# Performance work log

Hardware: AMD Instinct MI355X
Metric: run time of the kernel (lower is better)

The kernel has to match this reference:

```python
import jax, jax.numpy as jnp
import numpy as np

B, S, D, H = 2, 2048, 1024, 16
DH = D // H  # key_dim = embed_dim // num_heads
NEG = 1e9    # Keras masked-softmax adder magnitude
EPS = 1e-6


def setup_inputs() -> dict:
    key = jax.random.key(0)
    ks = jax.random.split(key, 6)
    sc = 1.0 / np.sqrt(D)
    return {
        "x": jax.random.normal(ks[0], (B, S, D), jnp.float32),
        "Wq": jax.random.normal(ks[1], (D, H, DH), jnp.float32) * sc,
        "bq": jnp.zeros((H, DH), jnp.float32),
        "Wk": jax.random.normal(ks[2], (D, H, DH), jnp.float32) * sc,
        "bk": jnp.zeros((H, DH), jnp.float32),
        "Wv": jax.random.normal(ks[3], (D, H, DH), jnp.float32) * sc,
        "bv": jnp.zeros((H, DH), jnp.float32),
        "Wo": jax.random.normal(ks[4], (H, DH, D), jnp.float32) * (1.0 / np.sqrt(D)),
        "bo": jnp.zeros((D,), jnp.float32),
        "gamma": jnp.ones((D,), jnp.float32),
        "beta": jnp.zeros((D,), jnp.float32),
    }


def reference(x, Wq, bq, Wk, bk, Wv, bv, Wo, bo, gamma, beta):
    # Keras MultiHeadAttention(query=x, value=x), inference (dropouts are identity)
    q = jnp.einsum("bsd,dhk->bshk", x, Wq) + bq  # [B,S,H,DH]
    k = jnp.einsum("bsd,dhk->bshk", x, Wk) + bk
    v = jnp.einsum("bsd,dhk->bshk", x, Wv) + bv

    scores = jnp.einsum("bqhd,bkhd->bhqk", q, k) / jnp.sqrt(jnp.asarray(DH, x.dtype))
    # Source: mask = 1 - band_part(ones, -1, 0) -> ones strictly ABOVE diagonal.
    # Keras attends where mask==1 and adds (1-mask)*(-1e9) elsewhere. Faithful:
    i = jnp.arange(S)[:, None]
    j = jnp.arange(S)[None, :]
    allowed = (j > i).astype(scores.dtype)  # [S,S], strict upper triangle
    scores = scores + (allowed - 1.0) * NEG  # subtract 1e9 where not allowed
    probs = jax.nn.softmax(scores, axis=-1)

    ctx = jnp.einsum("bhqk,bkhd->bqhd", probs, v)  # [B,S,H,DH]
    attn_out = jnp.einsum("bqhd,hdo->bqo", ctx, Wo) + bo  # [B,S,D]

    # residual + LayerNorm(eps=1e-6)
    y = x + attn_out
    mu = jnp.mean(y, axis=-1, keepdims=True)
    var = jnp.mean(jnp.square(y - mu), axis=-1, keepdims=True)
    return (y - mu) * jax.lax.rsqrt(var + EPS) * gamma + beta
```

## Files before the change

kernel.cpp:

```cpp
#include <hip/hip_runtime.h>
#include <hip/hip_bf16.h>

typedef __hip_bfloat16 bf16;
typedef __attribute__((ext_vector_type(8))) short bf16x8;
typedef __attribute__((ext_vector_type(4))) float f32x4;

constexpr int Bc  = 2;
constexpr int Sc  = 2048;
constexpr int Dc  = 1024;
constexpr int Hc  = 16;
constexpr int DHc = 64;
constexpr int BS  = Bc * Sc;
constexpr int NT  = Sc / 64;

__device__ __forceinline__ float bs2f(unsigned short u) {
    union { unsigned int i; float f; } v; v.i = ((unsigned int)u) << 16; return v.f;
}
__device__ __forceinline__ short f2bs(float x) {
    bf16 h = __float2bfloat16(x);
    return *reinterpret_cast<short*>(&h);
}

typedef const __attribute__((address_space(1))) unsigned int* as1_u32p;
typedef __attribute__((address_space(3))) unsigned int* as3_u32p;
__device__ __forceinline__ void gl_lds16(const void* g, void* l) {
    __builtin_amdgcn_global_load_lds((as1_u32p)g, (as3_u32p)l, 16, 0, 0);
}

__global__ __launch_bounds__(256) void cast_x(const float* __restrict__ in,
                                              short* __restrict__ out) {
    const int i = (blockIdx.x * 256 + threadIdx.x) * 4;
    const float4 v = *(const float4*)(in + i);
    ushort4 o;
    o.x = (unsigned short)f2bs(v.x);
    o.y = (unsigned short)f2bs(v.y);
    o.z = (unsigned short)f2bs(v.z);
    o.w = (unsigned short)f2bs(v.w);
    *(ushort4*)(out + i) = o;
}

__global__ __launch_bounds__(256) void transpose_cast(
    const float* __restrict__ w0, const float* __restrict__ w1,
    const float* __restrict__ w2, const float* __restrict__ w3,
    short* __restrict__ outbase)
{
    __shared__ float T[64][65];
    const int z = blockIdx.z;
    const float* in = (z == 0) ? w0 : (z == 1) ? w1 : (z == 2) ? w2 : w3;
    short* out = outbase + (size_t)z * 1024 * 1024;
    const int k0 = blockIdx.x * 64, n0 = blockIdx.y * 64;
    const int t = threadIdx.x;
    #pragma unroll
    for (int it = 0; it < 4; ++it) {
        const int s = it * 256 + t;
        const int r = s >> 4, c = (s & 15) * 4;
        *(float4*)&T[r][c] = *(const float4*)(in + (size_t)(k0 + r) * 1024 + n0 + c);
    }
    __syncthreads();
    #pragma unroll
    for (int it = 0; it < 4; ++it) {
        const int s = it * 256 + t;
        const int rr = s >> 4, cc = (s & 15) * 4;
        ushort4 o;
        o.x = (unsigned short)f2bs(T[cc + 0][rr]);
        o.y = (unsigned short)f2bs(T[cc + 1][rr]);
        o.z = (unsigned short)f2bs(T[cc + 2][rr]);
        o.w = (unsigned short)f2bs(T[cc + 3][rr]);
        *(ushort4*)(out + (size_t)(n0 + rr) * 1024 + k0 + cc) = o;
    }
}

__global__ __launch_bounds__(256, 2) void gemm_bt(
    const short* __restrict__ A, const short* __restrict__ BTbase,
    const float* __restrict__ b0, const float* __restrict__ b1,
    const float* __restrict__ b2, short* __restrict__ Cbase)
{
    __shared__ __align__(16) short As[128 * 64];
    __shared__ __align__(16) short Bs[128 * 64];

    const int z = blockIdx.z;
    const short* BT = BTbase + (size_t)z * 1024 * 1024;
    const float* bias = (z == 0) ? b0 : (z == 1) ? b1 : b2;
    short* C = Cbase + (size_t)z * BS * Dc;

    const int t = threadIdx.x;
    const int lane = t & 63, w = t >> 6;
    const int quad = lane >> 4, l16 = lane & 15;
    const int wm = (w & 1) * 64, wn = (w >> 1) * 64;
    const int row0 = blockIdx.y * 128;
    const int col0 = blockIdx.x * 128;
    const int sw = l16 & 7;

    f32x4 acc[4][4] = {};

    for (int kt = 0; kt < 1024; kt += 64) {
        __syncthreads();
        #pragma unroll
        for (int i = 0; i < 4; ++i) {
            const int f = i * 256 + t;
            const int r = f >> 3;
            const int g = (f & 7) ^ (r & 7);
            short* lb = &As[(i * 256 + w * 64) * 8];
            gl_lds16(A + (size_t)(row0 + r) * 1024 + kt + g * 8, lb);
            short* lb2 = &Bs[(i * 256 + w * 64) * 8];
            gl_lds16(BT + (size_t)(col0 + r) * 1024 + kt + g * 8, lb2);
        }
        __syncthreads();
        #pragma unroll
        for (int ks = 0; ks < 2; ++ks) {
            bf16x8 av[4], bv[4];
            #pragma unroll
            for (int mt = 0; mt < 4; ++mt) {
                const int r = wm + mt * 16 + l16;
                av[mt] = *(const bf16x8*)&As[r * 64 + ((ks * 4 + quad) ^ sw) * 8];
            }
            #pragma unroll
            for (int nt = 0; nt < 4; ++nt) {
                const int r = wn + nt * 16 + l16;
                bv[nt] = *(const bf16x8*)&Bs[r * 64 + ((ks * 4 + quad) ^ sw) * 8];
            }
            #pragma unroll
            for (int mt = 0; mt < 4; ++mt)
                #pragma unroll
                for (int nt = 0; nt < 4; ++nt)
                    acc[mt][nt] = __builtin_amdgcn_mfma_f32_16x16x32_bf16(
                        av[mt], bv[nt], acc[mt][nt], 0, 0, 0);
        }
    }

    float bvv[4];
    #pragma unroll
    for (int nt = 0; nt < 4; ++nt) bvv[nt] = bias[col0 + wn + nt * 16 + l16];
    #pragma unroll
    for (int mt = 0; mt < 4; ++mt)
        #pragma unroll
        for (int reg = 0; reg < 4; ++reg) {
            const size_t row = row0 + wm + mt * 16 + quad * 4 + reg;
            #pragma unroll
            for (int nt = 0; nt < 4; ++nt) {
                const int col = col0 + wn + nt * 16 + l16;
                C[row * 1024 + col] = f2bs(acc[mt][nt][reg] + bvv[nt]);
            }
        }
}

__device__ __forceinline__ void qtile_step(
    const bf16x8 (&qf)[2], const bf16x8 (&kf)[2][4],
    const short (&VsT)[64][72], short (&Psw)[16][72],
    const int k0, const int row_base,
    const int quad, const int l16,
    float (&l)[4], f32x4 (&O)[4])
{
    f32x4 S[4] = {};
    #pragma unroll
    for (int ks = 0; ks < 2; ++ks)
        #pragma unroll
        for (int nt = 0; nt < 4; ++nt)
            S[nt] = __builtin_amdgcn_mfma_f32_16x16x32_bf16(qf[ks], kf[ks][nt], S[nt], 0, 0, 0);

    #pragma unroll
    for (int nt = 0; nt < 4; ++nt) {
        const int col = k0 + nt * 16 + l16;
        #pragma unroll
        for (int reg = 0; reg < 4; ++reg) {
            const int row = row_base + quad * 4 + reg;
            const float s = (col > row) ? fminf(S[nt][reg] * 0.125f, 80.f) : -87.0f;
            const float p = __expf(s);
            S[nt][reg] = p;
            l[reg] += p;
        }
    }

    #pragma unroll
    for (int nt = 0; nt < 4; ++nt)
        #pragma unroll
        for (int reg = 0; reg < 4; ++reg)
            Psw[quad * 4 + reg][nt * 16 + l16] = f2bs(S[nt][reg]);

    #pragma unroll
    for (int ks = 0; ks < 2; ++ks) {
        const bf16x8 pf = *(const bf16x8*)&Psw[l16][ks * 32 + quad * 8];
        #pragma unroll
        for (int nt = 0; nt < 4; ++nt) {
            const bf16x8 vf = *(const bf16x8*)&VsT[nt * 16 + l16][ks * 32 + quad * 8];
            O[nt] = __builtin_amdgcn_mfma_f32_16x16x32_bf16(pf, vf, O[nt], 0, 0, 0);
        }
    }
}

__global__ __launch_bounds__(256, 2) void attn_mfma(
    const short* __restrict__ Qg, const short* __restrict__ Kg,
    const short* __restrict__ Vg, short* __restrict__ CTX)
{
    __shared__ __align__(16) short Ks [64][72];
    __shared__ __align__(16) short VsT[64][72];
    __shared__ __align__(16) short Ps[4][16][72];

    const int tid  = threadIdx.x;
    const int lane = tid & 63, w = tid >> 6;
    const int quad = lane >> 4, l16 = lane & 15;
    const int p  = blockIdx.x;
    const int h  = blockIdx.y;
    const int b  = blockIdx.z;
    const size_t rb = (size_t)b * Sc;
    const int cb = h * DHc;

    const int qa0 = p * 64;
    const int qb0 = (NT - 1 - p) * 64;
    const int tA0 = p;
    const int tB0 = NT - 1 - p;

    bf16x8 qfA[2], qfB[2];
    {
        const short* qa = Qg + (rb + qa0 + w * 16 + l16) * (size_t)Dc + cb + quad * 8;
        qfA[0] = *(const bf16x8*)(qa);
        qfA[1] = *(const bf16x8*)(qa + 32);
        const short* qb = Qg + (rb + qb0 + w * 16 + l16) * (size_t)Dc + cb + quad * 8;
        qfB[0] = *(const bf16x8*)(qb);
        qfB[1] = *(const bf16x8*)(qb + 32);
    }

    float lA[4] = {}, lB[4] = {};
    f32x4 OA[4] = {}, OB[4] = {};

    const int skey = tid & 63, sseg = (tid >> 6) * 16;

    {
        const size_t g = (rb + tA0 * 64 + skey) * (size_t)Dc + cb + sseg;
        const bf16x8 k0v = *(const bf16x8*)(Kg + g);
        const bf16x8 k1v = *(const bf16x8*)(Kg + g + 8);
        const bf16x8 v0v = *(const bf16x8*)(Vg + g);
        const bf16x8 v1v = *(const bf16x8*)(Vg + g + 8);
        *(bf16x8*)&Ks[skey][sseg]     = k0v;
        *(bf16x8*)&Ks[skey][sseg + 8] = k1v;
        #pragma unroll
        for (int e = 0; e < 8; ++e) {
            VsT[sseg + e][skey]     = v0v[e];
            VsT[sseg + 8 + e][skey] = v1v[e];
        }
    }
    __syncthreads();

    for (int t = tA0; t < NT; ++t) {
        const bool havenext = (t + 1 < NT);
        bf16x8 pk0, pk1, pv0, pv1;
        if (havenext) {
            const size_t g = (rb + (t + 1) * 64 + skey) * (size_t)Dc + cb + sseg;
            pk0 = *(const bf16x8*)(Kg + g);
            pk1 = *(const bf16x8*)(Kg + g + 8);
            pv0 = *(const bf16x8*)(Vg + g);
            pv1 = *(const bf16x8*)(Vg + g + 8);
        }

        const int k0 = t * 64;
        bf16x8 kf[2][4];
        #pragma unroll
        for (int ks = 0; ks < 2; ++ks)
            #pragma unroll
            for (int nt = 0; nt < 4; ++nt)
                kf[ks][nt] = *(const bf16x8*)&Ks[nt * 16 + l16][ks * 32 + quad * 8];

        qtile_step(qfA, kf, VsT, Ps[w], k0, qa0 + w * 16, quad, l16, lA, OA);
        if (t >= tB0)
            qtile_step(qfB, kf, VsT, Ps[w], k0, qb0 + w * 16, quad, l16, lB, OB);

        if (havenext) {
            __syncthreads();
            *(bf16x8*)&Ks[skey][sseg]     = pk0;
            *(bf16x8*)&Ks[skey][sseg + 8] = pk1;
            #pragma unroll
            for (int e = 0; e < 8; ++e) {
                VsT[sseg + e][skey]     = pv0[e];
                VsT[sseg + 8 + e][skey] = pv1[e];
            }
            __syncthreads();
        }
    }

    #pragma unroll
    for (int off = 1; off < 16; off <<= 1)
        #pragma unroll
        for (int reg = 0; reg < 4; ++reg) {
            lA[reg] += __shfl_xor(lA[reg], off, 64);
            lB[reg] += __shfl_xor(lB[reg], off, 64);
        }
    #pragma unroll
    for (int reg = 0; reg < 4; ++reg) { lA[reg] = 1.0f / lA[reg]; lB[reg] = 1.0f / lB[reg]; }
    #pragma unroll
    for (int nt = 0; nt < 4; ++nt)
        #pragma unroll
        for (int reg = 0; reg < 4; ++reg) {
            const size_t ra = rb + qa0 + w * 16 + quad * 4 + reg;
            CTX[ra * Dc + cb + nt * 16 + l16] = f2bs(OA[nt][reg] * lA[reg]);
            const size_t rbq = rb + qb0 + w * 16 + quad * 4 + reg;
            CTX[rbq * Dc + cb + nt * 16 + l16] = f2bs(OB[nt][reg] * lB[reg]);
        }
}

__global__ __launch_bounds__(256) void vmean(const short* __restrict__ V,
                                             short* __restrict__ CTX)
{
    const int h = blockIdx.x, b = blockIdx.y;
    const int t = threadIdx.x;
    const int dh = t & 63, ck = t >> 6;
    float s = 0.f;
    const short* vp = V + ((size_t)b * Sc + ck * 512) * Dc + h * DHc + dh;
    for (int j = 0; j < 512; ++j) s += bs2f(vp[(size_t)j * Dc]);
    __shared__ float red[4][64];
    red[ck][dh] = s;
    __syncthreads();
    if (ck == 0) {
        const float tot = (red[0][dh] + red[1][dh] + red[2][dh] + red[3][dh]) * (1.f / Sc);
        CTX[((size_t)b * Sc + Sc - 1) * Dc + h * DHc + dh] = f2bs(tot);
    }
}

__global__ __launch_bounds__(256, 4) void resid_ln(
    const float* __restrict__ X, const short* __restrict__ AO,
    const float* __restrict__ gamma, const float* __restrict__ beta,
    float* __restrict__ out)
{
    const int r = blockIdx.x;
    const int t = threadIdx.x;
    const size_t base = (size_t)r * Dc + t * 4;

    const float4 x4 = *(const float4*)(X + base);
    const ushort4 a4 = *(const ushort4*)(AO + base);
    float y[4];
    y[0] = x4.x + bs2f(a4.x);
    y[1] = x4.y + bs2f(a4.y);
    y[2] = x4.z + bs2f(a4.z);
    y[3] = x4.w + bs2f(a4.w);

    float s  = y[0] + y[1] + y[2] + y[3];
    float s2 = y[0]*y[0] + y[1]*y[1] + y[2]*y[2] + y[3]*y[3];
    #pragma unroll
    for (int off = 1; off < 64; off <<= 1) {
        s  += __shfl_xor(s,  off, 64);
        s2 += __shfl_xor(s2, off, 64);
    }
    __shared__ float red[8];
    const int w = t >> 6;
    if ((t & 63) == 0) { red[w] = s; red[4 + w] = s2; }
    __syncthreads();
    s  = red[0] + red[1] + red[2] + red[3];
    s2 = red[4] + red[5] + red[6] + red[7];

    const float mu   = s * (1.0f / Dc);
    const float rstd = rsqrtf(s2 * (1.0f / Dc) - mu * mu + 1e-6f);

    const float4 g4 = *(const float4*)(gamma + t * 4);
    const float4 b4 = *(const float4*)(beta  + t * 4);
    float4 o;
    o.x = (y[0] - mu) * rstd * g4.x + b4.x;
    o.y = (y[1] - mu) * rstd * g4.y + b4.y;
    o.z = (y[2] - mu) * rstd * g4.z + b4.z;
    o.w = (y[3] - mu) * rstd * g4.w + b4.w;
    *(float4*)(out + base) = o;
}

extern "C" void kernel_launch(void* const* d_in, const int* in_sizes, int n_in,
                              void* d_out, int out_size, void* d_ws, size_t ws_size,
                              hipStream_t stream)
{
    (void)in_sizes; (void)n_in; (void)out_size; (void)ws_size;
    const float* x     = (const float*)d_in[0];
    const float* Wq    = (const float*)d_in[1];
    const float* bq    = (const float*)d_in[2];
    const float* Wk    = (const float*)d_in[3];
    const float* bk    = (const float*)d_in[4];
    const float* Wv    = (const float*)d_in[5];
    const float* bv    = (const float*)d_in[6];
    const float* Wo    = (const float*)d_in[7];
    const float* bo    = (const float*)d_in[8];
    const float* gamma = (const float*)d_in[9];
    const float* beta  = (const float*)d_in[10];
    float* out = (float*)d_out;

    const size_t matN = (size_t)BS * Dc;
    const size_t wN   = (size_t)Dc * Dc;
    short* xb = (short*)d_ws;
    short* WT = xb + matN;
    short* Qb = WT + 4 * wN;
    short* Kb = Qb + matN;
    short* Vb = Kb + matN;
    short* Cx = Vb + matN;
    short* AO = Qb;

    cast_x<<<matN / 1024, 256, 0, stream>>>(x, xb);

    dim3 gt(16, 16, 4);
    transpose_cast<<<gt, 256, 0, stream>>>(Wq, Wk, Wv, Wo, WT);

    dim3 gq(Dc / 128, BS / 128, 3);
    gemm_bt<<<gq, 256, 0, stream>>>(xb, WT, bq, bk, bv, Qb);

    dim3 ga(16, Hc, Bc);
    attn_mfma<<<ga, 256, 0, stream>>>(Qb, Kb, Vb, Cx);

    dim3 gv(Hc, Bc);
    vmean<<<gv, 256, 0, stream>>>(Vb, Cx);

    dim3 go(Dc / 128, BS / 128, 1);
    gemm_bt<<<go, 256, 0, stream>>>(Cx, WT + 3 * wN, bo, bo, bo, AO);

    resid_ln<<<BS, 256, 0, stream>>>(x, AO, gamma, beta, out);
}
```

Before: 227.5 us.

## Split paired attention query tiles across 8 waves and raise GEMM occupancy hint

Result: no change. 225.2 us (-1.0%).

```diff
diff --git a/kernel.cpp b/kernel.cpp
--- a/kernel.cpp
+++ b/kernel.cpp
@@ -70,7 +70,7 @@
     }
 }
 
-__global__ __launch_bounds__(256, 2) void gemm_bt(
+__global__ __launch_bounds__(256, 3) void gemm_bt(
     const short* __restrict__ A, const short* __restrict__ BTbase,
     const float* __restrict__ b0, const float* __restrict__ b1,
     const float* __restrict__ b2, short* __restrict__ Cbase)
@@ -188,91 +188,74 @@
     }
 }
 
-__global__ __launch_bounds__(256, 2) void attn_mfma(
+__global__ __launch_bounds__(512, 4) void attn_mfma(
     const short* __restrict__ Qg, const short* __restrict__ Kg,
     const short* __restrict__ Vg, short* __restrict__ CTX)
 {
     __shared__ __align__(16) short Ks [64][72];
     __shared__ __align__(16) short VsT[64][72];
-    __shared__ __align__(16) short Ps[4][16][72];
+    __shared__ __align__(16) short Ps[8][16][72];
 
     const int tid  = threadIdx.x;
     const int lane = tid & 63, w = tid >> 6;
     const int quad = lane >> 4, l16 = lane & 15;
+    const int wq   = w & 3;
+    const bool isA = (w < 4);
     const int p  = blockIdx.x;
     const int h  = blockIdx.y;
     const int b  = blockIdx.z;
     const size_t rb = (size_t)b * Sc;
     const int cb = h * DHc;
 
-    const int qa0 = p * 64;
-    const int qb0 = (NT - 1 - p) * 64;
-    const int tA0 = p;
-    const int tB0 = NT - 1 - p;
-
-    bf16x8 qfA[2], qfB[2];
+    const int myT0 = isA ? p : (NT - 1 - p);
+    const int q0   = myT0 * 64;
+
+    bf16x8 qf[2];
     {
-        const short* qa = Qg + (rb + qa0 + w * 16 + l16) * (size_t)Dc + cb + quad * 8;
-        qfA[0] = *(const bf16x8*)(qa);
-        qfA[1] = *(const bf16x8*)(qa + 32);
-        const short* qb = Qg + (rb + qb0 + w * 16 + l16) * (size_t)Dc + cb + quad * 8;
-        qfB[0] = *(const bf16x8*)(qb);
-        qfB[1] = *(const bf16x8*)(qb + 32);
-    }
-
-    float lA[4] = {}, lB[4] = {};
-    f32x4 OA[4] = {}, OB[4] = {};
-
-    const int skey = tid & 63, sseg = (tid >> 6) * 16;
+        const short* qp = Qg + (rb + q0 + wq * 16 + l16) * (size_t)Dc + cb + quad * 8;
+        qf[0] = *(const bf16x8*)(qp);
+        qf[1] = *(const bf16x8*)(qp + 32);
+    }
+
+    float l[4] = {};
+    f32x4 O[4] = {};
+
+    const int skey = tid & 63, sseg = (tid >> 6) * 8;
 
     {
-        const size_t g = (rb + tA0 * 64 + skey) * (size_t)Dc + cb + sseg;
-        const bf16x8 k0v = *(const bf16x8*)(Kg + g);
-        const bf16x8 k1v = *(const bf16x8*)(Kg + g + 8);
-        const bf16x8 v0v = *(const bf16x8*)(Vg + g);
-        const bf16x8 v1v = *(const bf16x8*)(Vg + g + 8);
-        *(bf16x8*)&Ks[skey][sseg]     = k0v;
-        *(bf16x8*)&Ks[skey][sseg + 8] = k1v;
-        #pragma unroll
-        for (int e = 0; e < 8; ++e) {
-            VsT[sseg + e][skey]     = v0v[e];
-            VsT[sseg + 8 + e][skey] = v1v[e];
-        }
+        const size_t g = (rb + p * 64 + skey) * (size_t)Dc + cb + sseg;
+        const bf16x8 kv = *(const bf16x8*)(Kg + g);
+        const bf16x8 vv = *(const bf16x8*)(Vg + g);
+        *(bf16x8*)&Ks[skey][sseg] = kv;
+        #pragma unroll
+        for (int e = 0; e < 8; ++e) VsT[sseg + e][skey] = vv[e];
     }
     __syncthreads();
 
-    for (int t = tA0; t < NT; ++t) {
+    for (int t = p; t < NT; ++t) {
         const bool havenext = (t + 1 < NT);
-        bf16x8 pk0, pk1, pv0, pv1;
+        bf16x8 pk, pv;
         if (havenext) {
             const size_t g = (rb + (t + 1) * 64 + skey) * (size_t)Dc + cb + sseg;
-            pk0 = *(const bf16x8*)(Kg + g);
-            pk1 = *(const bf16x8*)(Kg + g + 8);
-            pv0 = *(const bf16x8*)(Vg + g);
-            pv1 = *(const bf16x8*)(Vg + g + 8);
-        }
-
-        const int k0 = t * 64;
-        bf16x8 kf[2][4];
-        #pragma unroll
-        for (int ks = 0; ks < 2; ++ks)
-            #pragma unroll
-            for (int nt = 0; nt < 4; ++nt)
-                kf[ks][nt] = *(const bf16x8*)&Ks[nt * 16 + l16][ks * 32 + quad * 8];
-
-        qtile_step(qfA, kf, VsT, Ps[w], k0, qa0 + w * 16, quad, l16, lA, OA);
-        if (t >= tB0)
-            qtile_step(qfB, kf, VsT, Ps[w], k0, qb0 + w * 16, quad, l16, lB, OB);
+            pk = *(const bf16x8*)(Kg + g);
+            pv = *(const bf16x8*)(Vg + g);
+        }
+
+        if (t >= myT0) {
+            bf16x8 kf[2][4];
+            #pragma unroll
+            for (int ks = 0; ks < 2; ++ks)
+                #pragma unroll
+                for (int nt = 0; nt < 4; ++nt)
+                    kf[ks][nt] = *(const bf16x8*)&Ks[nt * 16 + l16][ks * 32 + quad * 8];
+            qtile_step(qf, kf, VsT, Ps[w], t * 64, q0 + wq * 16, quad, l16, l, O);
+        }
 
         if (havenext) {
             __syncthreads();
-            *(bf16x8*)&Ks[skey][sseg]     = pk0;
-            *(bf16x8*)&Ks[skey][sseg + 8] = pk1;
-            #pragma unroll
-            for (int e = 0; e < 8; ++e) {
-                VsT[sseg + e][skey]     = pv0[e];
-                VsT[sseg + 8 + e][skey] = pv1[e];
-            }
+            *(bf16x8*)&Ks[skey][sseg] = pk;
+            #pragma unroll
+            for (int e = 0; e < 8; ++e) VsT[sseg + e][skey] = pv[e];
             __syncthreads();
         }
     }
@@ -280,20 +263,16 @@
     #pragma unroll
     for (int off = 1; off < 16; off <<= 1)
         #pragma unroll
+        for (int reg = 0; reg < 4; ++reg)
+            l[reg] += __shfl_xor(l[reg], off, 64);
+    #pragma unroll
+    for (int reg = 0; reg < 4; ++reg) l[reg] = 1.0f / l[reg];
+    #pragma unroll
+    for (int nt = 0; nt < 4; ++nt)
+        #pragma unroll
         for (int reg = 0; reg < 4; ++reg) {
-            lA[reg] += __shfl_xor(lA[reg], off, 64);
-            lB[reg] += __shfl_xor(lB[reg], off, 64);
-        }
-    #pragma unroll
-    for (int reg = 0; reg < 4; ++reg) { lA[reg] = 1.0f / lA[reg]; lB[reg] = 1.0f / lB[reg]; }
-    #pragma unroll
-    for (int nt = 0; nt < 4; ++nt)
-        #pragma unroll
-        for (int reg = 0; reg < 4; ++reg) {
-            const size_t ra = rb + qa0 + w * 16 + quad * 4 + reg;
-            CTX[ra * Dc + cb + nt * 16 + l16] = f2bs(OA[nt][reg] * lA[reg]);
-            const size_t rbq = rb + qb0 + w * 16 + quad * 4 + reg;
-            CTX[rbq * Dc + cb + nt * 16 + l16] = f2bs(OB[nt][reg] * lB[reg]);
+            const size_t row = rb + q0 + wq * 16 + quad * 4 + reg;
+            CTX[row * Dc + cb + nt * 16 + l16] = f2bs(O[nt][reg] * l[reg]);
         }
 }
 
@@ -396,7 +375,7 @@
     gemm_bt<<<gq, 256, 0, stream>>>(xb, WT, bq, bk, bv, Qb);
 
     dim3 ga(16, Hc, Bc);
-    attn_mfma<<<ga, 256, 0, stream>>>(Qb, Kb, Vb, Cx);
+    attn_mfma<<<ga, 512, 0, stream>>>(Qb, Kb, Vb, Cx);
 
     dim3 gv(Hc, Bc);
     vmean<<<gv, 256, 0, stream>>>(Vb, Cx);
```

## Split attention key range across two blocks and combine partial outputs

Applied to the files above, without the earlier changes.

Result: slower. 249.2 us (+9.6%).

```diff
diff --git a/kernel.cpp b/kernel.cpp
--- a/kernel.cpp
+++ b/kernel.cpp
@@ -70,7 +70,7 @@
     }
 }
 
-__global__ __launch_bounds__(256, 2) void gemm_bt(
+__global__ __launch_bounds__(256, 3) void gemm_bt(
     const short* __restrict__ A, const short* __restrict__ BTbase,
     const float* __restrict__ b0, const float* __restrict__ b1,
     const float* __restrict__ b2, short* __restrict__ Cbase)
@@ -188,9 +188,11 @@
     }
 }
 
-__global__ __launch_bounds__(256, 2) void attn_mfma(
+__global__ __launch_bounds__(256, 4) void attn_split(
     const short* __restrict__ Qg, const short* __restrict__ Kg,
-    const short* __restrict__ Vg, short* __restrict__ CTX)
+    const short* __restrict__ Vg,
+    short* __restrict__ Pa, short* __restrict__ Pb,
+    float* __restrict__ l0, float* __restrict__ l1)
 {
     __shared__ __align__(16) short Ks [64][72];
     __shared__ __align__(16) short VsT[64][72];
@@ -199,102 +201,120 @@
     const int tid  = threadIdx.x;
     const int lane = tid & 63, w = tid >> 6;
     const int quad = lane >> 4, l16 = lane & 15;
-    const int p  = blockIdx.x;
+    const int qs   = blockIdx.x >> 1;
+    const int half = blockIdx.x & 1;
     const int h  = blockIdx.y;
     const int b  = blockIdx.z;
     const size_t rb = (size_t)b * Sc;
     const int cb = h * DHc;
 
-    const int qa0 = p * 64;
-    const int qb0 = (NT - 1 - p) * 64;
-    const int tA0 = p;
-    const int tB0 = NT - 1 - p;
-
-    bf16x8 qfA[2], qfB[2];
+    const int q0 = qs * 64;
+    const int n  = NT - qs;
+    const int h0 = (n + 1) >> 1;
+    const int t_begin = half ? (qs + h0) : qs;
+    const int t_end   = half ? NT : (qs + h0);
+    short* Pout = half ? Pb : Pa;
+    float* lout = half ? l1 : l0;
+
+    bf16x8 qf[2];
     {
-        const short* qa = Qg + (rb + qa0 + w * 16 + l16) * (size_t)Dc + cb + quad * 8;
-        qfA[0] = *(const bf16x8*)(qa);
-        qfA[1] = *(const bf16x8*)(qa + 32);
-        const short* qb = Qg + (rb + qb0 + w * 16 + l16) * (size_t)Dc + cb + quad * 8;
-        qfB[0] = *(const bf16x8*)(qb);
-        qfB[1] = *(const bf16x8*)(qb + 32);
-    }
-
-    float lA[4] = {}, lB[4] = {};
-    f32x4 OA[4] = {}, OB[4] = {};
+        const short* qp = Qg + (rb + q0 + w * 16 + l16) * (size_t)Dc + cb + quad * 8;
+        qf[0] = *(const bf16x8*)(qp);
+        qf[1] = *(const bf16x8*)(qp + 32);
+    }
+
+    float l[4] = {};
+    f32x4 O[4] = {};
 
     const int skey = tid & 63, sseg = (tid >> 6) * 16;
 
-    {
-        const size_t g = (rb + tA0 * 64 + skey) * (size_t)Dc + cb + sseg;
-        const bf16x8 k0v = *(const bf16x8*)(Kg + g);
-        const bf16x8 k1v = *(const bf16x8*)(Kg + g + 8);
-        const bf16x8 v0v = *(const bf16x8*)(Vg + g);
-        const bf16x8 v1v = *(const bf16x8*)(Vg + g + 8);
-        *(bf16x8*)&Ks[skey][sseg]     = k0v;
-        *(bf16x8*)&Ks[skey][sseg + 8] = k1v;
-        #pragma unroll
-        for (int e = 0; e < 8; ++e) {
-            VsT[sseg + e][skey]     = v0v[e];
-            VsT[sseg + 8 + e][skey] = v1v[e];
-        }
-    }
-    __syncthreads();
-
-    for (int t = tA0; t < NT; ++t) {
-        const bool havenext = (t + 1 < NT);
-        bf16x8 pk0, pk1, pv0, pv1;
-        if (havenext) {
-            const size_t g = (rb + (t + 1) * 64 + skey) * (size_t)Dc + cb + sseg;
-            pk0 = *(const bf16x8*)(Kg + g);
-            pk1 = *(const bf16x8*)(Kg + g + 8);
-            pv0 = *(const bf16x8*)(Vg + g);
-            pv1 = *(const bf16x8*)(Vg + g + 8);
-        }
-
-        const int k0 = t * 64;
-        bf16x8 kf[2][4];
-        #pragma unroll
-        for (int ks = 0; ks < 2; ++ks)
-            #pragma unroll
-            for (int nt = 0; nt < 4; ++nt)
-                kf[ks][nt] = *(const bf16x8*)&Ks[nt * 16 + l16][ks * 32 + quad * 8];
-
-        qtile_step(qfA, kf, VsT, Ps[w], k0, qa0 + w * 16, quad, l16, lA, OA);
-        if (t >= tB0)
-            qtile_step(qfB, kf, VsT, Ps[w], k0, qb0 + w * 16, quad, l16, lB, OB);
-
-        if (havenext) {
-            __syncthreads();
-            *(bf16x8*)&Ks[skey][sseg]     = pk0;
-            *(bf16x8*)&Ks[skey][sseg + 8] = pk1;
+    if (t_begin < t_end) {
+        {
+            const size_t g = (rb + t_begin * 64 + skey) * (size_t)Dc + cb + sseg;
+            const bf16x8 k0v = *(const bf16x8*)(Kg + g);
+            const bf16x8 k1v = *(const bf16x8*)(Kg + g + 8);
+            const bf16x8 v0v = *(const bf16x8*)(Vg + g);
+            const bf16x8 v1v = *(const bf16x8*)(Vg + g + 8);
+            *(bf16x8*)&Ks[skey][sseg]     = k0v;
+            *(bf16x8*)&Ks[skey][sseg + 8] = k1v;
             #pragma unroll
             for (int e = 0; e < 8; ++e) {
-                VsT[sseg + e][skey]     = pv0[e];
-                VsT[sseg + 8 + e][skey] = pv1[e];
-            }
-            __syncthreads();
+                VsT[sseg + e][skey]     = v0v[e];
+                VsT[sseg + 8 + e][skey] = v1v[e];
+            }
+        }
+        __syncthreads();
+
+        for (int t = t_begin; t < t_end; ++t) {
+            const bool havenext = (t + 1 < t_end);
+            bf16x8 pk0, pk1, pv0, pv1;
+            if (havenext) {
+                const size_t g = (rb + (t + 1) * 64 + skey) * (size_t)Dc + cb + sseg;
+                pk0 = *(const bf16x8*)(Kg + g);
+                pk1 = *(const bf16x8*)(Kg + g + 8);
+                pv0 = *(const bf16x8*)(Vg + g);
+                pv1 = *(const bf16x8*)(Vg + g + 8);
+            }
+
+            bf16x8 kf[2][4];
+            #pragma unroll
+            for (int ks = 0; ks < 2; ++ks)
+                #pragma unroll
+                for (int nt = 0; nt < 4; ++nt)
+                    kf[ks][nt] = *(const bf16x8*)&Ks[nt * 16 + l16][ks * 32 + quad * 8];
+
+            qtile_step(qf, kf, VsT, Ps[w], t * 64, q0 + w * 16, quad, l16, l, O);
+
+            if (havenext) {
+                __syncthreads();
+                *(bf16x8*)&Ks[skey][sseg]     = pk0;
+                *(bf16x8*)&Ks[skey][sseg + 8] = pk1;
+                #pragma unroll
+                for (int e = 0; e < 8; ++e) {
+                    VsT[sseg + e][skey]     = pv0[e];
+                    VsT[sseg + 8 + e][skey] = pv1[e];
+                }
+                __syncthreads();
+            }
         }
     }
 
     #pragma unroll
     for (int off = 1; off < 16; off <<= 1)
         #pragma unroll
+        for (int reg = 0; reg < 4; ++reg)
+            l[reg] += __shfl_xor(l[reg], off, 64);
+
+    #pragma unroll
+    for (int nt = 0; nt < 4; ++nt)
+        #pragma unroll
         for (int reg = 0; reg < 4; ++reg) {
-            lA[reg] += __shfl_xor(lA[reg], off, 64);
-            lB[reg] += __shfl_xor(lB[reg], off, 64);
-        }
-    #pragma unroll
-    for (int reg = 0; reg < 4; ++reg) { lA[reg] = 1.0f / lA[reg]; lB[reg] = 1.0f / lB[reg]; }
-    #pragma unroll
-    for (int nt = 0; nt < 4; ++nt)
-        #pragma unroll
-        for (int reg = 0; reg < 4; ++reg) {
-            const size_t ra = rb + qa0 + w * 16 + quad * 4 + reg;
-            CTX[ra * Dc + cb + nt * 16 + l16] = f2bs(OA[nt][reg] * lA[reg]);
-            const size_t rbq = rb + qb0 + w * 16 + quad * 4 + reg;
-            CTX[rbq * Dc + cb + nt * 16 + l16] = f2bs(OB[nt][reg] * lB[reg]);
-        }
+            const size_t row = rb + q0 + w * 16 + quad * 4 + reg;
+            Pout[row * Dc + cb + nt * 16 + l16] = f2bs(O[nt][reg]);
+        }
+    if (l16 == 0)
+        #pragma unroll
+        for (int reg = 0; reg < 4; ++reg)
+            lout[(rb + q0 + w * 16 + quad * 4 + reg) * Hc + h] = l[reg];
+}
+
+__global__ __launch_bounds__(256) void combine(
+    short* __restrict__ Pa, const short* __restrict__ Pb,
+    const float* __restrict__ l0, const float* __restrict__ l1)
+{
+    const int r = blockIdx.x;
+    const int t = threadIdx.x;
+    const int c = t * 4;
+    const int h = t >> 4;
+    const float rl = 1.0f / (l0[(size_t)r * Hc + h] + l1[(size_t)r * Hc + h]);
+    const ushort4 a = *(const ushort4*)(Pa + (size_t)r * Dc + c);
+    const ushort4 bv = *(const ushort4*)(Pb + (size_t)r * Dc + c);
+    ushort4 o;
+    o.x = (unsigned short)f2bs((bs2f(a.x) + bs2f(bv.x)) * rl);
+    o.y = (unsigned short)f2bs((bs2f(a.y) + bs2f(bv.y)) * rl);
+    o.z = (unsigned short)f2bs((bs2f(a.z) + bs2f(bv.z)) * rl);
+    o.w = (unsigned short)f2bs((bs2f(a.w) + bs2f(bv.w)) * rl);
+    *(ushort4*)(Pa + (size_t)r * Dc + c) = o;
 }
 
 __global__ __launch_bounds__(256) void vmean(const short* __restrict__ V,
@@ -384,7 +404,10 @@
     short* Qb = WT + 4 * wN;
     short* Kb = Qb + matN;
     short* Vb = Kb + matN;
-    short* Cx = Vb + matN;
+    short* Pa = Vb + matN;
+    short* Pb = xb;
+    float* l0 = (float*)(Pa + matN);
+    float* l1 = l0 + (size_t)BS * Hc;
     short* AO = Qb;
 
     cast_x<<<matN / 1024, 256, 0, stream>>>(x, xb);
@@ -395,14 +418,16 @@
     dim3 gq(Dc / 128, BS / 128, 3);
     gemm_bt<<<gq, 256, 0, stream>>>(xb, WT, bq, bk, bv, Qb);
 
-    dim3 ga(16, Hc, Bc);
-    attn_mfma<<<ga, 256, 0, stream>>>(Qb, Kb, Vb, Cx);
+    dim3 ga(2 * NT, Hc, Bc);
+    attn_split<<<ga, 256, 0, stream>>>(Qb, Kb, Vb, Pa, Pb, l0, l1);
+
+    combine<<<BS, 256, 0, stream>>>(Pa, Pb, l0, l1);
 
     dim3 gv(Hc, Bc);
-    vmean<<<gv, 256, 0, stream>>>(Vb, Cx);
+    vmean<<<gv, 256, 0, stream>>>(Vb, Pa);
 
     dim3 go(Dc / 128, BS / 128, 1);
-    gemm_bt<<<go, 256, 0, stream>>>(Cx, WT + 3 * wN, bo, bo, bo, AO);
+    gemm_bt<<<go, 256, 0, stream>>>(Pa, WT + 3 * wN, bo, bo, bo, AO);
 
     resid_ln<<<BS, 256, 0, stream>>>(x, AO, gamma, beta, out);
 }
```

## Give each attention wave 32 contiguous query rows and fold the softmax scale into Q

Applied to the files above, without the earlier changes.

After: 239.3 us. 5.2% more time.

```diff
diff --git a/kernel.cpp b/kernel.cpp
--- a/kernel.cpp
+++ b/kernel.cpp
@@ -70,10 +70,11 @@
     }
 }
 
-__global__ __launch_bounds__(256, 2) void gemm_bt(
+__global__ __launch_bounds__(256, 3) void gemm_bt(
     const short* __restrict__ A, const short* __restrict__ BTbase,
     const float* __restrict__ b0, const float* __restrict__ b1,
-    const float* __restrict__ b2, short* __restrict__ Cbase)
+    const float* __restrict__ b2, short* __restrict__ Cbase,
+    const float qsc)
 {
     __shared__ __align__(16) short As[128 * 64];
     __shared__ __align__(16) short Bs[128 * 64];
@@ -81,6 +82,7 @@
     const int z = blockIdx.z;
     const short* BT = BTbase + (size_t)z * 1024 * 1024;
     const float* bias = (z == 0) ? b0 : (z == 1) ? b1 : b2;
+    const float osc = (z == 0) ? qsc : 1.0f;
     short* C = Cbase + (size_t)z * BS * Dc;
 
     const int t = threadIdx.x;
@@ -139,53 +141,9 @@
             #pragma unroll
             for (int nt = 0; nt < 4; ++nt) {
                 const int col = col0 + wn + nt * 16 + l16;
-                C[row * 1024 + col] = f2bs(acc[mt][nt][reg] + bvv[nt]);
-            }
-        }
-}
-
-__device__ __forceinline__ void qtile_step(
-    const bf16x8 (&qf)[2], const bf16x8 (&kf)[2][4],
-    const short (&VsT)[64][72], short (&Psw)[16][72],
-    const int k0, const int row_base,
-    const int quad, const int l16,
-    float (&l)[4], f32x4 (&O)[4])
-{
-    f32x4 S[4] = {};
-    #pragma unroll
-    for (int ks = 0; ks < 2; ++ks)
-        #pragma unroll
-        for (int nt = 0; nt < 4; ++nt)
-            S[nt] = __builtin_amdgcn_mfma_f32_16x16x32_bf16(qf[ks], kf[ks][nt], S[nt], 0, 0, 0);
-
-    #pragma unroll
-    for (int nt = 0; nt < 4; ++nt) {
-        const int col = k0 + nt * 16 + l16;
-        #pragma unroll
-        for (int reg = 0; reg < 4; ++reg) {
-            const int row = row_base + quad * 4 + reg;
-            const float s = (col > row) ? fminf(S[nt][reg] * 0.125f, 80.f) : -87.0f;
-            const float p = __expf(s);
-            S[nt][reg] = p;
-            l[reg] += p;
-        }
-    }
-
-    #pragma unroll
-    for (int nt = 0; nt < 4; ++nt)
-        #pragma unroll
-        for (int reg = 0; reg < 4; ++reg)
-            Psw[quad * 4 + reg][nt * 16 + l16] = f2bs(S[nt][reg]);
-
-    #pragma unroll
-    for (int ks = 0; ks < 2; ++ks) {
-        const bf16x8 pf = *(const bf16x8*)&Psw[l16][ks * 32 + quad * 8];
-        #pragma unroll
-        for (int nt = 0; nt < 4; ++nt) {
-            const bf16x8 vf = *(const bf16x8*)&VsT[nt * 16 + l16][ks * 32 + quad * 8];
-            O[nt] = __builtin_amdgcn_mfma_f32_16x16x32_bf16(pf, vf, O[nt], 0, 0, 0);
-        }
-    }
+                C[row * 1024 + col] = f2bs((acc[mt][nt][reg] + bvv[nt]) * osc);
+            }
+        }
 }
 
 __global__ __launch_bounds__(256, 2) void attn_mfma(
@@ -194,39 +152,35 @@
 {
     __shared__ __align__(16) short Ks [64][72];
     __shared__ __align__(16) short VsT[64][72];
-    __shared__ __align__(16) short Ps[4][16][72];
+    __shared__ __align__(16) short Ps[4][32][72];
 
     const int tid  = threadIdx.x;
     const int lane = tid & 63, w = tid >> 6;
     const int quad = lane >> 4, l16 = lane & 15;
-    const int p  = blockIdx.x;
+    const int qb = blockIdx.x ^ (blockIdx.z ? 15 : 0);
     const int h  = blockIdx.y;
     const int b  = blockIdx.z;
     const size_t rb = (size_t)b * Sc;
     const int cb = h * DHc;
 
-    const int qa0 = p * 64;
-    const int qb0 = (NT - 1 - p) * 64;
-    const int tA0 = p;
-    const int tB0 = NT - 1 - p;
-
-    bf16x8 qfA[2], qfB[2];
+    const int q0 = qb * 128 + w * 32;
+    const int t0 = qb * 2;
+
+    bf16x8 qf[2][2];
+    #pragma unroll
+    for (int mt = 0; mt < 2; ++mt) {
+        const short* qp = Qg + (rb + q0 + mt * 16 + l16) * (size_t)Dc + cb + quad * 8;
+        qf[mt][0] = *(const bf16x8*)(qp);
+        qf[mt][1] = *(const bf16x8*)(qp + 32);
+    }
+
+    float l[2][4] = {};
+    f32x4 O[2][4] = {};
+
+    const int skey = tid & 63, sseg = (tid >> 6) * 16;
+
     {
-        const short* qa = Qg + (rb + qa0 + w * 16 + l16) * (size_t)Dc + cb + quad * 8;
-        qfA[0] = *(const bf16x8*)(qa);
-        qfA[1] = *(const bf16x8*)(qa + 32);
-        const short* qb = Qg + (rb + qb0 + w * 16 + l16) * (size_t)Dc + cb + quad * 8;
-        qfB[0] = *(const bf16x8*)(qb);
-        qfB[1] = *(const bf16x8*)(qb + 32);
-    }
-
-    float lA[4] = {}, lB[4] = {};
-    f32x4 OA[4] = {}, OB[4] = {};
-
-    const int skey = tid & 63, sseg = (tid >> 6) * 16;
-
-    {
-        const size_t g = (rb + tA0 * 64 + skey) * (size_t)Dc + cb + sseg;
+        const size_t g = (rb + t0 * 64 + skey) * (size_t)Dc + cb + sseg;
         const bf16x8 k0v = *(const bf16x8*)(Kg + g);
         const bf16x8 k1v = *(const bf16x8*)(Kg + g + 8);
         const bf16x8 v0v = *(const bf16x8*)(Vg + g);
@@ -241,7 +195,7 @@
     }
     __syncthreads();
 
-    for (int t = tA0; t < NT; ++t) {
+    for (int t = t0; t < NT; ++t) {
         const bool havenext = (t + 1 < NT);
         bf16x8 pk0, pk1, pv0, pv1;
         if (havenext) {
@@ -252,7 +206,6 @@
             pv1 = *(const bf16x8*)(Vg + g + 8);
         }
 
-        const int k0 = t * 64;
         bf16x8 kf[2][4];
         #pragma unroll
         for (int ks = 0; ks < 2; ++ks)
@@ -260,9 +213,45 @@
             for (int nt = 0; nt < 4; ++nt)
                 kf[ks][nt] = *(const bf16x8*)&Ks[nt * 16 + l16][ks * 32 + quad * 8];
 
-        qtile_step(qfA, kf, VsT, Ps[w], k0, qa0 + w * 16, quad, l16, lA, OA);
-        if (t >= tB0)
-            qtile_step(qfB, kf, VsT, Ps[w], k0, qb0 + w * 16, quad, l16, lB, OB);
+        f32x4 S[2][4] = {};
+        #pragma unroll
+        for (int ks = 0; ks < 2; ++ks)
+            #pragma unroll
+            for (int nt = 0; nt < 4; ++nt) {
+                S[0][nt] = __builtin_amdgcn_mfma_f32_16x16x32_bf16(qf[0][ks], kf[ks][nt], S[0][nt], 0, 0, 0);
+                S[1][nt] = __builtin_amdgcn_mfma_f32_16x16x32_bf16(qf[1][ks], kf[ks][nt], S[1][nt], 0, 0, 0);
+            }
+
+        #pragma unroll
+        for (int mt = 0; mt < 2; ++mt)
+            #pragma unroll
+            for (int nt = 0; nt < 4; ++nt) {
+                const int col = t * 64 + nt * 16 + l16;
+                #pragma unroll
+                for (int reg = 0; reg < 4; ++reg) {
+                    const int row = q0 + mt * 16 + quad * 4 + reg;
+                    const float p = (col > row)
+                        ? __expf(fminf(S[mt][nt][reg], 80.f)) : 0.f;
+                    l[mt][reg] += p;
+                    Ps[w][mt * 16 + quad * 4 + reg][nt * 16 + l16] = f2bs(p);
+                }
+            }
+
+        bf16x8 vf[2][4];
+        #pragma unroll
+        for (int ks = 0; ks < 2; ++ks)
+            #pragma unroll
+            for (int nt = 0; nt < 4; ++nt)
+                vf[ks][nt] = *(const bf16x8*)&VsT[nt * 16 + l16][ks * 32 + quad * 8];
+        #pragma unroll
+        for (int mt = 0; mt < 2; ++mt)
+            #pragma unroll
+            for (int ks = 0; ks < 2; ++ks) {
+                const bf16x8 pf = *(const bf16x8*)&Ps[w][mt * 16 + l16][ks * 32 + quad * 8];
+                #pragma unroll
+                for (int nt = 0; nt < 4; ++nt)
+                    O[mt][nt] = __builtin_amdgcn_mfma_f32_16x16x32_bf16(pf, vf[ks][nt], O[mt][nt], 0, 0, 0);
+            }
 
         if (havenext) {
             __syncthreads();
@@ -280,21 +269,24 @@
     #pragma unroll
     for (int off = 1; off < 16; off <<= 1)
         #pragma unroll
-        for (int reg = 0; reg < 4; ++reg) {
-            lA[reg] += __shfl_xor(lA[reg], off, 64);
-            lB[reg] += __shfl_xor(lB[reg], off, 64);
-        }
-    #pragma unroll
-    for (int reg = 0; reg < 4; ++reg) { lA[reg] = 1.0f / lA[reg]; lB[reg] = 1.0f / lB[reg]; }
-    #pragma unroll
-    for (int nt = 0; nt < 4; ++nt)
-        #pragma unroll
-        for (int reg = 0; reg < 4; ++reg) {
-            const size_t ra = rb + qa0 + w * 16 + quad * 4 + reg;
-            CTX[ra * Dc + cb + nt * 16 + l16] = f2bs(OA[nt][reg] * lA[reg]);
-            const size_t rbq = rb + qb0 + w * 16 + quad * 4 + reg;
-            CTX[rbq * Dc + cb + nt * 16 + l16] = f2bs(OB[nt][reg] * lB[reg]);
-        }
+        for (int mt = 0; mt < 2; ++mt)
+            #pragma unroll
+            for (int reg = 0; reg < 4; ++reg)
+                l[mt][reg] += __shfl_xor(l[mt][reg], off, 64);
+    #pragma unroll
+    for (int mt = 0; mt < 2; ++mt)
+        #pragma unroll
+        for (int reg = 0; reg < 4; ++reg)
+            l[mt][reg] = 1.0f / l[mt][reg];
+    #pragma unroll
+    for (int mt = 0; mt < 2; ++mt)
+        #pragma unroll
+        for (int nt = 0; nt < 4; ++nt)
+            #pragma unroll
+            for (int reg = 0; reg < 4; ++reg) {
+                const size_t row = rb + q0 + mt * 16 + quad * 4 + reg;
+                CTX[row * Dc + cb + nt * 16 + l16] = f2bs(O[mt][nt][reg] * l[mt][reg]);
+            }
 }
 
 __global__ __launch_bounds__(256) void vmean(const short* __restrict__ V,
@@ -393,7 +385,7 @@
     transpose_cast<<<gt, 256, 0, stream>>>(Wq, Wk, Wv, Wo, WT);
 
     dim3 gq(Dc / 128, BS / 128, 3);
-    gemm_bt<<<gq, 256, 0, stream>>>(xb, WT, bq, bk, bv, Qb);
+    gemm_bt<<<gq, 256, 0, stream>>>(xb, WT, bq, bk, bv, Qb, 0.125f);
 
     dim3 ga(16, Hc, Bc);
     attn_mfma<<<ga, 256, 0, stream>>>(Qb, Kb, Vb, Cx);
@@ -402,7 +394,7 @@
     vmean<<<gv, 256, 0, stream>>>(Vb, Cx);
 
     dim3 go(Dc / 128, BS / 128, 1);
-    gemm_bt<<<go, 256, 0, stream>>>(Cx, WT + 3 * wN, bo, bo, bo, AO);
+    gemm_bt<<<go, 256, 0, stream>>>(Cx, WT + 3 * wN, bo, bo, bo, AO, 1.0f);
 
     resid_ln<<<BS, 256, 0, stream>>>(x, AO, gamma, beta, out);
 }
```
